# Kernel optimization log

Measured on AMD Instinct MI355X. Metric: run time of the kernel, lower is better.

## Reference

```python
import jax, jax.numpy as jnp
import numpy as np

HIDDEN = 256
TOPK = 16
SINK_BLOCKS = 5
TAU = 1.0
SOFT_ALPHA = 8.0
LN_EPS = 1e-5


def setup_inputs() -> dict:
    key = jax.random.key(0)
    ks = jax.random.split(key, 8)
    B, T, QD, KD, J = 2, 1024, 1024, 1024, 64
    H = HIDDEN
    H3 = 3 * H
    s = 0.02
    return {
        "Q": jax.random.normal(ks[0], (B, T, QD), dtype=jnp.float32),
        "K": jax.random.normal(ks[1], (B, J, KD), dtype=jnp.float32),
        "Wq": jax.random.normal(ks[2], (H, QD), dtype=jnp.float32) * s,
        "Wk": jax.random.normal(ks[3], (H, KD), dtype=jnp.float32) * s,
        "ln_g": jnp.ones((H3,), dtype=jnp.float32),
        "ln_b": jnp.zeros((H3,), dtype=jnp.float32),
        "Wu": jax.random.normal(ks[4], (H, H3), dtype=jnp.float32) * s,
        "bu": jnp.zeros((H,), dtype=jnp.float32),
        "Wv": jax.random.normal(ks[5], (H, H3), dtype=jnp.float32) * s,
        "bv": jnp.zeros((H,), dtype=jnp.float32),
        "Wo": jax.random.normal(ks[6], (1, H), dtype=jnp.float32) * s,
        "bo": jnp.zeros((1,), dtype=jnp.float32),
        "chunk_len": 16,
        "L_ctx": 1024,
    }


def _forward(Q, K, Wq, Wk, ln_g, ln_b, Wu, bu, Wv, bv, Wo, bo, chunk_len, L_ctx):
    B, T, _ = Q.shape
    J = K.shape[1]
    # ---- GatedScorer ----
    q = jnp.einsum('btd,hd->bth', Q, Wq)  # (B,T,H)
    k = jnp.einsum('bjd,hd->bjh', K, Wk)  # (B,J,H)
    H = q.shape[-1]
    qb = jnp.broadcast_to(q[:, :, None, :], (B, T, J, H))
    kb = jnp.broadcast_to(k[:, None, :, :], (B, T, J, H))
    x = jnp.concatenate([qb, kb, qb * kb], axis=-1)  # (B,T,J,3H)
    mu = jnp.mean(x, axis=-1, keepdims=True)
    var = jnp.mean((x - mu) ** 2, axis=-1, keepdims=True)
    x = (x - mu) / jnp.sqrt(var + LN_EPS) * ln_g + ln_b
    U = jnp.einsum('btjc,hc->btjh', x, Wu) + bu
    V = jnp.einsum('btjc,hc->btjh', x, Wv) + bv
    Z = U * jax.nn.gelu(V, approximate=False)
    logits = jnp.einsum('btjh,oh->btjo', Z, Wo)[..., 0] + bo[0]  # (B,T,J)

    # ---- top-k chunk selection (deterministic path, use_learnable_k=False) ----
    sink = int(min(max(0, SINK_BLOCKS), J))
    J_tail = J - sink
    topk_main = max(min(J, TOPK) - sink, 0)
    logits_tail = logits[..., sink:]  # (B,T,J_tail)
    causal = jnp.arange(J_tail)[None, :] <= jnp.arange(T)[:, None]  # tril(T,J_tail)
    masked = jnp.where(causal[None], logits_tail, -jnp.inf)
    _, idx_tail = jax.lax.top_k(masked, topk_main)
    idx_tail = idx_tail + sink
    sink_idx = jnp.broadcast_to(jnp.arange(sink)[None, None, :], (B, T, sink))
    idx = jnp.concatenate([sink_idx, idx_tail], axis=-1)  # (B,T,sink+topk_main)

    # ---- soft warmup weights ----
    w_soft = jax.nn.softmax(logits / TAU, axis=-1)  # (B,T,J)

    # ---- build_block_bias_from_topk ----
    num_chunks = (L_ctx + chunk_len - 1) // chunk_len
    sel = jnp.zeros((B, T, num_chunks), dtype=bool)
    sel = sel.at[jnp.arange(B)[:, None, None], jnp.arange(T)[None, :, None], idx].set(True)
    token_chunk = jnp.clip(jnp.arange(L_ctx) // chunk_len, 0, num_chunks - 1)  # (L_ctx,)
    sel_tok = jnp.take(sel, token_chunk, axis=-1)  # (B,T,L_ctx)
    per_chunk_bias = -SOFT_ALPHA * (1.0 - w_soft)  # (B,T,J)
    bias = jnp.take(per_chunk_bias, token_chunk, axis=-1)  # (B,T,L_ctx)
    bias = jnp.where(sel_tok, 0.0, bias)
    tri = jnp.arange(L_ctx)[None, :] > jnp.arange(T)[:, None]  # triu(T,L_ctx, diag=1)
    bias = jnp.where(tri[None], -jnp.inf, bias)
    return logits, bias


def reference(Q, K, Wq, Wk, ln_g, ln_b, Wu, bu, Wv, bv, Wo, bo, chunk_len, L_ctx):
    return _forward(Q, K, Wq, Wk, ln_g, ln_b, Wu, bu, Wv, bv, Wo, bo, chunk_len, L_ctx)
```

## Files before the change

kernel.cpp:

```cpp
#include <hip/hip_runtime.h>
#include <hip/hip_bf16.h>
#include <math.h>

#define H3 768

#define OFF_Q     0u
#define OFF_K     524288u
#define OFF_UVK   557056u
#define OFF_SQP   622592u
#define OFF_SQ2P  640000u
#define OFF_WGU   657408u
#define OFF_WGV   657664u
#define OFF_CU    657920u
#define OFF_CV    658176u

#define BO_UVQ   0u
#define BO_WQF   1048576u
#define BO_WKF   1310720u
#define BO_BPK   1572864u
#define BO_WQBF  1703936u
#define BO_WKBF  1835008u

typedef __attribute__((ext_vector_type(8))) short bf16x8;
typedef __attribute__((ext_vector_type(4))) float f32x4;

__device__ __forceinline__ float bf2f(short s) {
    return __uint_as_float(((unsigned)(unsigned short)s) << 16);
}
union bfu { __hip_bfloat162 h; short2 s; };
__device__ __forceinline__ void split2(float a, float b, short* hi2, short* lo2) {
    bfu h; h.h = __float22bfloat162_rn(float2{a, b});
    float fa = bf2f(h.s.x), fb = bf2f(h.s.y);
    bfu l; l.h = __float22bfloat162_rn(float2{a - fa, b - fb});
    hi2[0] = h.s.x; hi2[1] = h.s.y;
    lo2[0] = l.s.x; lo2[1] = l.s.y;
}
__device__ __forceinline__ void split8(const float* v, bf16x8* vh, bf16x8* vl) {
    short h2[2], l2[2];
#pragma unroll
    for (int i = 0; i < 4; i++) {
        split2(v[2 * i], v[2 * i + 1], h2, l2);
        (*vh)[2 * i] = h2[0]; (*vh)[2 * i + 1] = h2[1];
        (*vl)[2 * i] = l2[0]; (*vl)[2 * i + 1] = l2[1];
    }
}

__device__ __forceinline__ float gelu_fast(float v) {
    float ar = v * 0.70710678118654752440f;
    float a = fabsf(ar);
    float t = __builtin_amdgcn_rcpf(fmaf(0.3275911f, a, 1.0f));
    float p = fmaf(fmaf(fmaf(fmaf(1.061405429f, t, -1.453152027f), t,
                             1.421413741f), t, -0.284496736f), t, 0.254829592f) * t;
    float e = __expf(-ar * ar);
    float er = fmaf(-p, e, 1.0f);
    er = copysignf(er, ar);
    return 0.5f * v * (1.0f + er);
}

__device__ __forceinline__ float wave_reduce_add(float v) {
#pragma unroll
    for (int off = 32; off > 0; off >>= 1) v += __shfl_xor(v, off, 64);
    return v;
}

__global__ __launch_bounds__(256) void prep(const float* __restrict__ Wq,
                                            const float* __restrict__ Wk,
                                            const float* __restrict__ Wu,
                                            const float* __restrict__ Wv,
                                            const float* __restrict__ g,
                                            const float* __restrict__ lb,
                                            const float* __restrict__ bu,
                                            const float* __restrict__ bv,
                                            float* __restrict__ ws,
                                            float* __restrict__ bsc) {
    int tid = threadIdx.x;
    int bid = blockIdx.x;
    if (bid < 64) {
        int h = bid * 4 + (tid >> 6);
        int lane = tid & 63;
        float su = 0.f, sv = 0.f, tu = 0.f, tv = 0.f;
#pragma unroll
        for (int i = 0; i < 12; i++) {
            int c = lane + 64 * i;
            float gg = g[c], bb = lb[c];
            float wu = Wu[h * H3 + c], wv = Wv[h * H3 + c];
            su += wu * gg; sv += wv * gg; tu += wu * bb; tv += wv * bb;
        }
        su = wave_reduce_add(su); sv = wave_reduce_add(sv);
        tu = wave_reduce_add(tu); tv = wave_reduce_add(tv);
        if (lane == 0) {
            ws[OFF_WGU + h] = su; ws[OFF_WGV + h] = sv;
            ws[OFF_CU + h] = tu + bu[h]; ws[OFF_CV + h] = tv + bv[h];
        }
        return;
    }
    float v8[8];
    bf16x8 vh, vl;
    if (bid < 320) {
        const float* W; bf16x8* dst;
        int idx;
        if (bid < 192) { idx = (bid - 64) * 256 + tid; W = Wq; dst = (bf16x8*)(bsc + BO_WQF); }
        else { idx = (bid - 192) * 256 + tid; W = Wk; dst = (bf16x8*)(bsc + BO_WKF); }
        int n = idx >> 7, k8 = idx & 127;
        const float* src = W + (size_t)n * 1024 + k8 * 8;
        *(float4*)&v8[0] = *(const float4*)src;
        *(float4*)&v8[4] = *(const float4*)(src + 4);
        split8(v8, &vh, &vl);
        int kc = k8 >> 2, grp = k8 & 3, lane = grp * 16 + (n & 15), ntg = n >> 4;
        size_t s0 = ((size_t)(kc * 16 + ntg) * 2) * 64 + lane;
        dst[s0] = vh; dst[s0 + 64] = vl;
        return;
    }
    int idx, c0;
    bf16x8* dst;
    int n;
    if (bid < 384) {
        idx = (bid - 320) * 256 + tid;
        n = idx >> 5; c0 = (idx & 31) * 8;
        dst = (bf16x8*)(bsc + BO_WQBF);
    } else if (bid < 448) {
        idx = (bid - 384) * 256 + tid;
        n = idx >> 5; c0 = 256 + (idx & 31) * 8;
        dst = (bf16x8*)(bsc + BO_WKBF);
    } else {
        idx = (bid - 448) * 256 + tid;
        n = idx >> 5; c0 = 512 + (idx & 31) * 8;
        dst = (bf16x8*)(bsc + BO_BPK);
    }
    int h, uv;
    if (bid < 448) { uv = (n < 256) ? 0 : 1; h = (n < 256) ? n : n - 256; }
    else {
        int ntg0 = n >> 4, cc = n & 15;
        uv = ntg0 & 1;
        h = ((ntg0 >> 3) << 6) | (((ntg0 >> 1) & 3) << 4) | cc;
    }
    const float* W = uv ? Wv : Wu;
#pragma unroll
    for (int i = 0; i < 8; i++) v8[i] = W[(size_t)h * H3 + c0 + i] * g[c0 + i];
    split8(v8, &vh, &vl);
    int k8 = (c0 & 255) >> 3;
    int kc = k8 >> 2, grp = k8 & 3, lane = grp * 16 + (n & 15), ntg = n >> 4;
    size_t s0 = ((size_t)(kc * 32 + ntg) * 2) * 64 + lane;
    dst[s0] = vh; dst[s0 + 64] = vl;
}

__global__ __launch_bounds__(256) void proj_mfma(const float* __restrict__ Q,
                                                 const float* __restrict__ Kin,
                                                 const float* __restrict__ bsc,
                                                 float* __restrict__ ws) {
    __shared__ __align__(16) short Ah[32 * 40], Al[32 * 40];
    int tid = threadIdx.x, bx = blockIdx.x, by = blockIdx.y;
    const float* A; float* C; const bf16x8* BF; int sbase;
    if (by < 64) {
        A = Q + (size_t)by * 32 * 1024;
        C = ws + OFF_Q + (size_t)by * 32 * 256;
        BF = (const bf16x8*)(bsc + BO_WQF);
        sbase = by * 32;
    } else {
        A = Kin + (size_t)(by - 64) * 32 * 1024;
        C = ws + OFF_K + (size_t)(by - 64) * 32 * 256;
        BF = (const bf16x8*)(bsc + BO_WKF);
        sbase = 2048 + (by - 64) * 32;
    }
    int w = tid >> 6, l = tid & 63, c15 = l & 15, grp = l >> 4;
    int mt = w & 1, np = w >> 1;
    int srow = tid >> 3, scol = (tid & 7) * 4;
    f32x4 acc[2];
    acc[0] = (f32x4){0.f, 0.f, 0.f, 0.f};
    acc[1] = (f32x4){0.f, 0.f, 0.f, 0.f};
    for (int kc = 0; kc < 32; kc++) {
        float4 a4 = *(const float4*)&A[(size_t)srow * 1024 + kc * 32 + scol];
        short h4[4], l4[4];
        split2(a4.x, a4.y, &h4[0], &l4[0]);
        split2(a4.z, a4.w, &h4[2], &l4[2]);
        int ao = srow * 40 + scol;
        *(short4*)&Ah[ao] = *(short4*)&h4[0];
        *(short4*)&Al[ao] = *(short4*)&l4[0];
        __syncthreads();
        int fo = (mt * 16 + c15) * 40 + grp * 8;
        bf16x8 afh = *(const bf16x8*)&Ah[fo];
        bf16x8 afl = *(const bf16x8*)&Al[fo];
        bf16x8 bh[2], bl[2];
#pragma unroll
        for (int i = 0; i < 2; i++) {
            int ntg = bx * 4 + 2 * np + i;
            size_t fi = ((size_t)(kc * 16 + ntg) * 2) * 64 + l;
            bh[i] = BF[fi]; bl[i] = BF[fi + 64];
        }
#pragma unroll
        for (int i = 0; i < 2; i++)
            acc[i] = __builtin_amdgcn_mfma_f32_16x16x32_bf16(afl, bh[i], acc[i], 0, 0, 0);
#pragma unroll
        for (int i = 0; i < 2; i++)
            acc[i] = __builtin_amdgcn_mfma_f32_16x16x32_bf16(afh, bl[i], acc[i], 0, 0, 0);
#pragma unroll
        for (int i = 0; i < 2; i++)
            acc[i] = __builtin_amdgcn_mfma_f32_16x16x32_bf16(afh, bh[i], acc[i], 0, 0, 0);
        __syncthreads();
    }
#pragma unroll
    for (int r = 0; r < 4; r++) {
        int rloc = mt * 16 + grp * 4 + r;
#pragma unroll
        for (int i = 0; i < 2; i++)
            C[(size_t)rloc * 256 + bx * 64 + (2 * np + i) * 16 + c15] = acc[i][r];
        float s = acc[0][r] + acc[1][r];
        float sq = acc[0][r] * acc[0][r] + acc[1][r] * acc[1][r];
#pragma unroll
        for (int off = 1; off <= 8; off <<= 1) {
            s += __shfl_xor(s, off, 64);
            sq += __shfl_xor(sq, off, 64);
        }
        if (c15 == 0) {
            int nb = bx * 2 + np;
            ws[OFF_SQP + nb * 2176 + sbase + rloc] = s;
            ws[OFF_SQ2P + nb * 2176 + sbase + rloc] = sq;
        }
    }
}

__global__ __launch_bounds__(256) void uv_mfma(const float* __restrict__ ws_ro,
                                               float* __restrict__ ws,
                                               float* __restrict__ bsc) {
    __shared__ __align__(16) short Ah[64 * 40], Al[64 * 40];
    int tid = threadIdx.x, bx = blockIdx.x, by = blockIdx.y;
    const float* A; float* C; const bf16x8* BF;
    if (by < 32) {
        A = ws_ro + OFF_Q + (size_t)by * 64 * 256;
        C = bsc + BO_UVQ + (size_t)by * 64 * 512;
        BF = (const bf16x8*)(bsc + BO_WQBF);
    } else {
        A = ws_ro + OFF_K + (size_t)(by - 32) * 64 * 256;
        C = ws + OFF_UVK + (size_t)(by - 32) * 64 * 512;
        BF = (const bf16x8*)(bsc + BO_WKBF);
    }
    int w = tid >> 6, l = tid & 63, c15 = l & 15, grp = l >> 4;
    int srow = tid >> 2, scol = (tid & 3) * 8;
    f32x4 acc[4];
#pragma unroll
    for (int nt = 0; nt < 4; nt++) acc[nt] = (f32x4){0.f, 0.f, 0.f, 0.f};
    for (int kc = 0; kc < 8; kc++) {
        float v8[8];
        const float* src = &A[(size_t)srow * 256 + kc * 32 + scol];
        *(float4*)&v8[0] = *(const float4*)src;
        *(float4*)&v8[4] = *(const float4*)(src + 4);
        bf16x8 vh, vl;
        split8(v8, &vh, &vl);
        int ao = srow * 40 + scol;
        *(bf16x8*)&Ah[ao] = vh;
        *(bf16x8*)&Al[ao] = vl;
        __syncthreads();
        int fo = (w * 16 + c15) * 40 + grp * 8;
        bf16x8 afh = *(const bf16x8*)&Ah[fo];
        bf16x8 afl = *(const bf16x8*)&Al[fo];
        bf16x8 bh[4], bl[4];
#pragma unroll
        for (int nt = 0; nt < 4; nt++) {
            int ntg = bx * 4 + nt;
            size_t fi = ((size_t)(kc * 32 + ntg) * 2) * 64 + l;
            bh[nt] = BF[fi]; bl[nt] = BF[fi + 64];
        }
#pragma unroll
        for (int nt = 0; nt < 4; nt++)
            acc[nt] = __builtin_amdgcn_mfma_f32_16x16x32_bf16(afl, bh[nt], acc[nt], 0, 0, 0);
#pragma unroll
        for (int nt = 0; nt < 4; nt++)
            acc[nt] = __builtin_amdgcn_mfma_f32_16x16x32_bf16(afh, bl[nt], acc[nt], 0, 0, 0);
#pragma unroll
        for (int nt = 0; nt < 4; nt++)
            acc[nt] = __builtin_amdgcn_mfma_f32_16x16x32_bf16(afh, bh[nt], acc[nt], 0, 0, 0);
        __syncthreads();
    }
#pragma unroll
    for (int nt = 0; nt < 4; nt++)
#pragma unroll
        for (int r = 0; r < 4; r++)
            C[(size_t)(w * 16 + grp * 4 + r) * 512 + bx * 64 + nt * 16 + c15] = acc[nt][r];
}

__global__ __launch_bounds__(512, 4) void main_mfma(const float* __restrict__ ws,
                                                    const float* __restrict__ bsc,
                                                    const float* __restrict__ Wo,
                                                    const float* __restrict__ bo,
                                                    float* __restrict__ logits) {
    __shared__ float kk[256];
    __shared__ __align__(16) short Ah[4][64 * 40];
    __shared__ __align__(16) short Al[4][64 * 40];
    __shared__ float mu_s[64], inv_s[64];
    __shared__ float part_s[8][64];
    int tid = threadIdx.x;
    int t0 = blockIdx.x << 6;
    int j = blockIdx.y, b = blockIdx.z;
    int bj = (b << 6) | j;
    if (tid < 256) kk[tid] = ws[OFF_K + bj * 256 + tid];
    int w = tid >> 6, l = tid & 63, c15 = l & 15, grp = l >> 4;
    int srow = tid >> 3, scol = (tid & 7) * 4;
    const float* qrow = ws + OFF_Q + (size_t)((b << 10) + t0 + srow) * 256;
    const bf16x8* bpk = (const bf16x8*)(bsc + BO_BPK);
    const float* UVQ = bsc + BO_UVQ;
    f32x4 acc[4][4];
#pragma unroll
    for (int mt = 0; mt < 4; mt++)
#pragma unroll
        for (int nt = 0; nt < 4; nt++) acc[mt][nt] = (f32x4){0.f, 0.f, 0.f, 0.f};
    float s1 = 0.f, s2 = 0.f;
    __syncthreads();
#pragma unroll
    for (int p = 0; p < 2; p++) {
#pragma unroll
        for (int kc = 0; kc < 4; kc++) {
            int kcg = p * 4 + kc;
            float4 q4 = *(const float4*)&qrow[kcg * 32 + scol];
            float4 k4 = *(const float4*)&kk[kcg * 32 + scol];
            float a0 = q4.x * k4.x, a1 = q4.y * k4.y;
            float a2 = q4.z * k4.z, a3 = q4.w * k4.w;
            s1 += (a0 + a1) + (a2 + a3);
            s2 = fmaf(a0, a0, s2); s2 = fmaf(a1, a1, s2);
            s2 = fmaf(a2, a2, s2); s2 = fmaf(a3, a3, s2);
            short h4[4], l4[4];
            split2(a0, a1, &h4[0], &l4[0]);
            split2(a2, a3, &h4[2], &l4[2]);
            int ao = srow * 40 + scol;
            *(short4*)&Ah[kc][ao] = *(short4*)&h4[0];
            *(short4*)&Al[kc][ao] = *(short4*)&l4[0];
        }
        if (p == 1) {
            s1 += __shfl_xor(s1, 1, 64); s1 += __shfl_xor(s1, 2, 64); s1 += __shfl_xor(s1, 4, 64);
            s2 += __shfl_xor(s2, 1, 64); s2 += __shfl_xor(s2, 2, 64); s2 += __shfl_xor(s2, 4, 64);
            if ((tid & 7) == 0) {
                int row = (b << 10) + t0 + srow;
                float sq = s1, sq2 = s2;
#pragma unroll
                for (int nb = 0; nb < 8; nb++) {
                    sq += ws[OFF_SQP + nb * 2176 + row] + ws[OFF_SQP + nb * 2176 + 2048 + bj];
                    sq2 += ws[OFF_SQ2P + nb * 2176 + row] + ws[OFF_SQ2P + nb * 2176 + 2048 + bj];
                }
                float muv = sq * (1.0f / 768.0f);
                float ex2 = sq2 * (1.0f / 768.0f);
                mu_s[srow] = muv;
                inv_s[srow] = 1.0f / sqrtf(ex2 - muv * muv + 1e-5f);
            }
        }
        __syncthreads();
#pragma unroll
        for (int kc = 0; kc < 4; kc++) {
            int kcg = p * 4 + kc;
            bf16x8 afh[4], afl[4];
#pragma unroll
            for (int mt = 0; mt < 4; mt++) {
                int ao = (mt * 16 + c15) * 40 + grp * 8;
                afh[mt] = *(const bf16x8*)&Ah[kc][ao];
                afl[mt] = *(const bf16x8*)&Al[kc][ao];
            }
#pragma unroll
            for (int nt = 0; nt < 4; nt++) {
                int ntg = w * 4 + nt;
                size_t fi = ((size_t)(kcg * 32 + ntg) * 2) * 64 + l;
                bf16x8 bh = bpk[fi];
                bf16x8 bl = bpk[fi + 64];
#pragma unroll
                for (int mt = 0; mt < 4; mt++)
                    acc[mt][nt] = __builtin_amdgcn_mfma_f32_16x16x32_bf16(afl[mt], bh, acc[mt][nt], 0, 0, 0);
#pragma unroll
                for (int mt = 0; mt < 4; mt++)
                    acc[mt][nt] = __builtin_amdgcn_mfma_f32_16x16x32_bf16(afh[mt], bl, acc[mt][nt], 0, 0, 0);
#pragma unroll
                for (int mt = 0; mt < 4; mt++)
                    acc[mt][nt] = __builtin_amdgcn_mfma_f32_16x16x32_bf16(afh[mt], bh, acc[mt][nt], 0, 0, 0);
            }
        }
        if (p == 0) __syncthreads();
    }
    float wgu_r[2], wgv_r[2], cu_r[2], cv_r[2], wo_r[2], uk_r[2], vk_r[2];
    int h2[2];
#pragma unroll
    for (int a = 0; a < 2; a++) {
        int ntg = 4 * w + 2 * a;
        int h = ((ntg >> 3) << 6) | (((ntg >> 1) & 3) << 4) | c15;
        h2[a] = h;
        wgu_r[a] = ws[OFF_WGU + h]; wgv_r[a] = ws[OFF_WGV + h];
        cu_r[a] = ws[OFF_CU + h]; cv_r[a] = ws[OFF_CV + h];
        wo_r[a] = Wo[h];
        uk_r[a] = ws[OFF_UVK + (size_t)bj * 512 + h];
        vk_r[a] = ws[OFF_UVK + (size_t)bj * 512 + 256 + h];
    }
#pragma unroll
    for (int mt = 0; mt < 4; mt++) {
#pragma unroll
        for (int r4 = 0; r4 < 4; r4++) {
            int r = mt * 16 + grp * 4 + r4;
            int row = (b << 10) + t0 + r;
            float muv = mu_s[r], invv = inv_s[r];
            const float* uvq = UVQ + (size_t)row * 512;
            float part = 0.f;
#pragma unroll
            for (int a = 0; a < 2; a++) {
                float U = invv * (acc[mt][2 * a][r4] + uvq[h2[a]] + uk_r[a] - muv * wgu_r[a]) + cu_r[a];
                float V = invv * (acc[mt][2 * a + 1][r4] + uvq[256 + h2[a]] + vk_r[a] - muv * wgv_r[a]) + cv_r[a];
                part = fmaf(wo_r[a] * U, gelu_fast(V), part);
            }
            part += __shfl_xor(part, 1, 64);
            part += __shfl_xor(part, 2, 64);
            part += __shfl_xor(part, 4, 64);
            part += __shfl_xor(part, 8, 64);
            if (c15 == 0) part_s[w][r] = part;
        }
    }
    __syncthreads();
    if (tid < 64) {
        float v = bo[0];
#pragma unroll
        for (int ww = 0; ww < 8; ww++) v += part_s[ww][tid];
        logits[(size_t)((b << 10) + t0 + tid) * 64 + j] = v;
    }
}

__global__ __launch_bounds__(256) void topk_bias(const float* __restrict__ logits,
                                                 float* __restrict__ bias,
                                                 const int* __restrict__ p_cl,
                                                 const int* __restrict__ p_L) {
    int wv = threadIdx.x >> 6, lane = threadIdx.x & 63;
    int row = blockIdx.x * 4 + wv;
    int t = row & 1023;
    __shared__ float pcb[4][64];
    float L = logits[(size_t)row * 64 + lane];
    float mx = L;
#pragma unroll
    for (int off = 32; off > 0; off >>= 1) mx = fmaxf(mx, __shfl_xor(mx, off, 64));
    float e = expf(L - mx);
    float s = wave_reduce_add(e);
    pcb[wv][lane] = -8.0f * (1.0f - e / s);
    bool valid = (lane >= 5) && ((lane - 5) <= t);
    float val = (lane >= 5) ? (valid ? L : -INFINITY) : -INFINITY;
    int idv = (lane >= 5) ? lane : (1 << 28);
    unsigned long long selmask = 0x1Full;
    for (int it = 0; it < 11; it++) {
        float bv = val; int bi = idv;
#pragma unroll
        for (int off = 32; off > 0; off >>= 1) {
            float ov = __shfl_xor(bv, off, 64);
            int oi = __shfl_xor(bi, off, 64);
            if (ov > bv || (ov == bv && oi < bi)) { bv = ov; bi = oi; }
        }
        selmask |= 1ull << bi;
        if (lane == bi) { val = -INFINITY; idv = (1 << 27); }
    }
    int clen = p_cl[0], Lctx = p_L[0];
    int nch1 = (Lctx + clen - 1) / clen - 1;
    float* brow = bias + (size_t)row * Lctx;
    if ((Lctx & 3) == 0) {
        float4* brow4 = (float4*)brow;
        for (int q = lane; q < (Lctx >> 2); q += 64) {
            float o[4];
#pragma unroll
            for (int i = 0; i < 4; i++) {
                int ll = 4 * q + i;
                int c = min(min((unsigned)ll / (unsigned)clen, (unsigned)nch1), 63u);
                float v;
                if (ll > t) v = -1e30f;
                else if ((selmask >> c) & 1ull) v = 0.0f;
                else v = pcb[wv][c];
                o[i] = v;
            }
            brow4[q] = *(float4*)&o[0];
        }
    } else {
        for (int ll = lane; ll < Lctx; ll += 64) {
            int c = min(min((unsigned)ll / (unsigned)clen, (unsigned)nch1), 63u);
            float v;
            if (ll > t) v = -1e30f;
            else if ((selmask >> c) & 1ull) v = 0.0f;
            else v = pcb[wv][c];
            brow[ll] = v;
        }
    }
}

extern "C" void kernel_launch(void* const* d_in, const int* in_sizes, int n_in,
                              void* d_out, int out_size, void* d_ws, size_t ws_size,
                              hipStream_t stream) {
    const float* Q   = (const float*)d_in[0];
    const float* Kin = (const float*)d_in[1];
    const float* Wq  = (const float*)d_in[2];
    const float* Wk  = (const float*)d_in[3];
    const float* g   = (const float*)d_in[4];
    const float* lb  = (const float*)d_in[5];
    const float* Wu  = (const float*)d_in[6];
    const float* bu  = (const float*)d_in[7];
    const float* Wv  = (const float*)d_in[8];
    const float* bv  = (const float*)d_in[9];
    const float* Wo  = (const float*)d_in[10];
    const float* bo  = (const float*)d_in[11];
    const int* p_cl  = (const int*)d_in[12];
    const int* p_L   = (const int*)d_in[13];
    float* ws = (float*)d_ws;
    float* logits = (float*)d_out;
    float* bias = (float*)d_out + (size_t)2 * 1024 * 64;

    prep<<<512, 256, 0, stream>>>(Wq, Wk, Wu, Wv, g, lb, bu, bv, ws, bias);
    proj_mfma<<<dim3(4, 68), 256, 0, stream>>>(Q, Kin, bias, ws);
    uv_mfma<<<dim3(8, 34), 256, 0, stream>>>(ws, ws, bias);
    main_mfma<<<dim3(16, 64, 2), 512, 0, stream>>>(ws, bias, Wo, bo, logits);
    topk_bias<<<512, 256, 0, stream>>>(logits, bias, p_cl, p_L);
}
```

Measured before the change: 264.1 us.

## Split-K projection with atomics, double-buffer LDS, relocate LN stats, swizzle main grid

The Q/K projection is split along K into two halves. Each half accumulates into the output with atomicAdd, so `prep` gets extra blocks that zero the output first. The projection loop now double-buffers its LDS tiles and prefetches the next A tile into registers, which removes one barrier per iteration. Row sum and sum-of-squares statistics move from the projection epilogue into `uv_mfma`, so `main_mfma` reads one value instead of eight partials. `main_mfma` also uses a 1D grid with a swizzled tile order, likely to improve L2 reuse. The costs are atomic traffic, the extra zeroing pass, and a redundant stats pass in the first `uv_mfma` column of blocks.

```diff
diff --git a/kernel.cpp b/kernel.cpp
--- a/kernel.cpp
+++ b/kernel.cpp
@@ -7,12 +7,12 @@
 #define OFF_Q     0u
 #define OFF_K     524288u
 #define OFF_UVK   557056u
-#define OFF_SQP   622592u
-#define OFF_SQ2P  640000u
-#define OFF_WGU   657408u
-#define OFF_WGV   657664u
-#define OFF_CU    657920u
-#define OFF_CV    658176u
+#define OFF_SQ    622592u
+#define OFF_SQ2   624768u
+#define OFF_WGU   626944u
+#define OFF_WGV   627200u
+#define OFF_CU    627456u
+#define OFF_CV    627712u
 
 #define BO_UVQ   0u
 #define BO_WQF   1048576u
@@ -75,6 +75,10 @@
                                             float* __restrict__ bsc) {
     int tid = threadIdx.x;
     int bid = blockIdx.x;
+    if (bid >= 512) {
+        ws[(bid - 512) * 256 + tid] = 0.0f;
+        return;
+    }
     if (bid < 64) {
         int h = bid * 4 + (tid >> 6);
         int lane = tid & 63;
@@ -148,43 +152,45 @@
                                                  const float* __restrict__ Kin,
                                                  const float* __restrict__ bsc,
                                                  float* __restrict__ ws) {
-    __shared__ __align__(16) short Ah[32 * 40], Al[32 * 40];
-    int tid = threadIdx.x, bx = blockIdx.x, by = blockIdx.y;
-    const float* A; float* C; const bf16x8* BF; int sbase;
+    __shared__ __align__(16) short Ah[2][32 * 40], Al[2][32 * 40];
+    int tid = threadIdx.x, bx = blockIdx.x, by = blockIdx.y, ks = blockIdx.z;
+    const float* A; float* C; const bf16x8* BF;
     if (by < 64) {
         A = Q + (size_t)by * 32 * 1024;
         C = ws + OFF_Q + (size_t)by * 32 * 256;
         BF = (const bf16x8*)(bsc + BO_WQF);
-        sbase = by * 32;
     } else {
         A = Kin + (size_t)(by - 64) * 32 * 1024;
         C = ws + OFF_K + (size_t)(by - 64) * 32 * 256;
         BF = (const bf16x8*)(bsc + BO_WKF);
-        sbase = 2048 + (by - 64) * 32;
     }
     int w = tid >> 6, l = tid & 63, c15 = l & 15, grp = l >> 4;
     int mt = w & 1, np = w >> 1;
     int srow = tid >> 3, scol = (tid & 7) * 4;
+    const float* arow = A + (size_t)srow * 1024 + ks * 512 + scol;
     f32x4 acc[2];
     acc[0] = (f32x4){0.f, 0.f, 0.f, 0.f};
     acc[1] = (f32x4){0.f, 0.f, 0.f, 0.f};
-    for (int kc = 0; kc < 32; kc++) {
-        float4 a4 = *(const float4*)&A[(size_t)srow * 1024 + kc * 32 + scol];
+    float4 a4 = *(const float4*)&arow[0];
+    for (int kc = 0; kc < 16; kc++) {
+        int pb = kc & 1;
         short h4[4], l4[4];
         split2(a4.x, a4.y, &h4[0], &l4[0]);
         split2(a4.z, a4.w, &h4[2], &l4[2]);
         int ao = srow * 40 + scol;
-        *(short4*)&Ah[ao] = *(short4*)&h4[0];
-        *(short4*)&Al[ao] = *(short4*)&l4[0];
+        *(short4*)&Ah[pb][ao] = *(short4*)&h4[0];
+        *(short4*)&Al[pb][ao] = *(short4*)&l4[0];
+        if (kc < 15) a4 = *(const float4*)&arow[(kc + 1) * 32];
         __syncthreads();
         int fo = (mt * 16 + c15) * 40 + grp * 8;
-        bf16x8 afh = *(const bf16x8*)&Ah[fo];
-        bf16x8 afl = *(const bf16x8*)&Al[fo];
+        bf16x8 afh = *(const bf16x8*)&Ah[pb][fo];
+        bf16x8 afl = *(const bf16x8*)&Al[pb][fo];
+        int kcg = ks * 16 + kc;
         bf16x8 bh[2], bl[2];
 #pragma unroll
         for (int i = 0; i < 2; i++) {
             int ntg = bx * 4 + 2 * np + i;
-            size_t fi = ((size_t)(kc * 16 + ntg) * 2) * 64 + l;
+            size_t fi = ((size_t)(kcg * 16 + ntg) * 2) * 64 + l;
             bh[i] = BF[fi]; bl[i] = BF[fi + 64];
         }
 #pragma unroll
@@ -196,54 +202,47 @@
 #pragma unroll
         for (int i = 0; i < 2; i++)
             acc[i] = __builtin_amdgcn_mfma_f32_16x16x32_bf16(afh, bh[i], acc[i], 0, 0, 0);
-        __syncthreads();
     }
 #pragma unroll
     for (int r = 0; r < 4; r++) {
         int rloc = mt * 16 + grp * 4 + r;
 #pragma unroll
         for (int i = 0; i < 2; i++)
-            C[(size_t)rloc * 256 + bx * 64 + (2 * np + i) * 16 + c15] = acc[i][r];
-        float s = acc[0][r] + acc[1][r];
-        float sq = acc[0][r] * acc[0][r] + acc[1][r] * acc[1][r];
-#pragma unroll
-        for (int off = 1; off <= 8; off <<= 1) {
-            s += __shfl_xor(s, off, 64);
-            sq += __shfl_xor(sq, off, 64);
-        }
-        if (c15 == 0) {
-            int nb = bx * 2 + np;
-            ws[OFF_SQP + nb * 2176 + sbase + rloc] = s;
-            ws[OFF_SQ2P + nb * 2176 + sbase + rloc] = sq;
-        }
-    }
-}
-
-__global__ __launch_bounds__(256) void uv_mfma(const float* __restrict__ ws_ro,
-                                               float* __restrict__ ws,
+            atomicAdd(&C[(size_t)rloc * 256 + bx * 64 + (2 * np + i) * 16 + c15], acc[i][r]);
+    }
+}
+
+__global__ __launch_bounds__(256) void uv_mfma(float* __restrict__ ws,
                                                float* __restrict__ bsc) {
     __shared__ __align__(16) short Ah[64 * 40], Al[64 * 40];
     int tid = threadIdx.x, bx = blockIdx.x, by = blockIdx.y;
-    const float* A; float* C; const bf16x8* BF;
+    const float* A; float* C; const bf16x8* BF; int sbase;
     if (by < 32) {
-        A = ws_ro + OFF_Q + (size_t)by * 64 * 256;
+        A = ws + OFF_Q + (size_t)by * 64 * 256;
         C = bsc + BO_UVQ + (size_t)by * 64 * 512;
         BF = (const bf16x8*)(bsc + BO_WQBF);
+        sbase = by * 64;
     } else {
-        A = ws_ro + OFF_K + (size_t)(by - 32) * 64 * 256;
+        A = ws + OFF_K + (size_t)(by - 32) * 64 * 256;
         C = ws + OFF_UVK + (size_t)(by - 32) * 64 * 512;
         BF = (const bf16x8*)(bsc + BO_WKBF);
+        sbase = 2048 + (by - 32) * 64;
     }
     int w = tid >> 6, l = tid & 63, c15 = l & 15, grp = l >> 4;
     int srow = tid >> 2, scol = (tid & 3) * 8;
     f32x4 acc[4];
 #pragma unroll
     for (int nt = 0; nt < 4; nt++) acc[nt] = (f32x4){0.f, 0.f, 0.f, 0.f};
+    float s1 = 0.f, s2 = 0.f;
     for (int kc = 0; kc < 8; kc++) {
         float v8[8];
         const float* src = &A[(size_t)srow * 256 + kc * 32 + scol];
         *(float4*)&v8[0] = *(const float4*)src;
         *(float4*)&v8[4] = *(const float4*)(src + 4);
+        if (bx == 0) {
+#pragma unroll
+            for (int i = 0; i < 8; i++) { s1 += v8[i]; s2 = fmaf(v8[i], v8[i], s2); }
+        }
         bf16x8 vh, vl;
         split8(v8, &vh, &vl);
         int ao = srow * 40 + scol;
@@ -270,6 +269,14 @@
         for (int nt = 0; nt < 4; nt++)
             acc[nt] = __builtin_amdgcn_mfma_f32_16x16x32_bf16(afh, bh[nt], acc[nt], 0, 0, 0);
         __syncthreads();
+    }
+    if (bx == 0) {
+        s1 += __shfl_xor(s1, 1, 64); s1 += __shfl_xor(s1, 2, 64);
+        s2 += __shfl_xor(s2, 1, 64); s2 += __shfl_xor(s2, 2, 64);
+        if ((tid & 3) == 0) {
+            ws[OFF_SQ + sbase + srow] = s1;
+            ws[OFF_SQ2 + sbase + srow] = s2;
+        }
     }
 #pragma unroll
     for (int nt = 0; nt < 4; nt++)
@@ -289,8 +296,11 @@
     __shared__ float mu_s[64], inv_s[64];
     __shared__ float part_s[8][64];
     int tid = threadIdx.x;
-    int t0 = blockIdx.x << 6;
-    int j = blockIdx.y, b = blockIdx.z;
+    int bidf = blockIdx.x;
+    int ti = ((bidf & 7) << 1) | ((bidf >> 3) & 1);
+    int j = (bidf >> 4) & 63;
+    int b = bidf >> 10;
+    int t0 = ti << 6;
     int bj = (b << 6) | j;
     if (tid < 256) kk[tid] = ws[OFF_K + bj * 256 + tid];
     int w = tid >> 6, l = tid & 63, c15 = l & 15, grp = l >> 4;
@@ -329,12 +339,8 @@
             s2 += __shfl_xor(s2, 1, 64); s2 += __shfl_xor(s2, 2, 64); s2 += __shfl_xor(s2, 4, 64);
             if ((tid & 7) == 0) {
                 int row = (b << 10) + t0 + srow;
-                float sq = s1, sq2 = s2;
-#pragma unroll
-                for (int nb = 0; nb < 8; nb++) {
-                    sq += ws[OFF_SQP + nb * 2176 + row] + ws[OFF_SQP + nb * 2176 + 2048 + bj];
-                    sq2 += ws[OFF_SQ2P + nb * 2176 + row] + ws[OFF_SQ2P + nb * 2176 + 2048 + bj];
-                }
+                float sq = s1 + ws[OFF_SQ + row] + ws[OFF_SQ + 2048 + bj];
+                float sq2 = s2 + ws[OFF_SQ2 + row] + ws[OFF_SQ2 + 2048 + bj];
                 float muv = sq * (1.0f / 768.0f);
                 float ex2 = sq2 * (1.0f / 768.0f);
                 mu_s[srow] = muv;
@@ -497,9 +503,9 @@
     float* logits = (float*)d_out;
     float* bias = (float*)d_out + (size_t)2 * 1024 * 64;
 
-    prep<<<512, 256, 0, stream>>>(Wq, Wk, Wu, Wv, g, lb, bu, bv, ws, bias);
-    proj_mfma<<<dim3(4, 68), 256, 0, stream>>>(Q, Kin, bias, ws);
-    uv_mfma<<<dim3(8, 34), 256, 0, stream>>>(ws, ws, bias);
-    main_mfma<<<dim3(16, 64, 2), 512, 0, stream>>>(ws, bias, Wo, bo, logits);
+    prep<<<2688, 256, 0, stream>>>(Wq, Wk, Wu, Wv, g, lb, bu, bv, ws, bias);
+    proj_mfma<<<dim3(4, 68, 2), 256, 0, stream>>>(Q, Kin, bias, ws);
+    uv_mfma<<<dim3(8, 34), 256, 0, stream>>>(ws, bias);
+    main_mfma<<<2048, 512, 0, stream>>>(ws, bias, Wo, bo, logits);
     topk_bias<<<512, 256, 0, stream>>>(logits, bias, p_cl, p_L);
 }
```

After: 249.5 us. -5.5%, faster.
